# Performance work log

Measured on AMD Instinct MI355X. Metric: run time of the kernel, lower is better.

## Reference

```python
import math
import jax, jax.numpy as jnp
import numpy as np


def _alibi_slopes(n):
    def pow2_slopes(n):
        start = 2.0 ** (-(2.0 ** (-(math.log2(n) - 3))))
        return [start * (start ** i) for i in range(n)]
    if math.log2(n).is_integer():
        return pow2_slopes(n)
    cp2 = 2 ** math.floor(math.log2(n))
    return pow2_slopes(cp2) + _alibi_slopes(2 * cp2)[0::2][: n - cp2]


NUM_HEADS = 16


def setup_inputs() -> dict:
    key = jax.random.key(0)
    ks = jax.random.split(key, 5)
    B, S, H = 2, 2048, 2048
    return {
        "hidden_states": jax.random.normal(ks[0], (B, S, H), jnp.float32),
        "w_qkv": jax.random.normal(ks[1], (H, 3 * H), jnp.float32) * (H ** -0.5),
        "b_qkv": jax.random.normal(ks[2], (3 * H,), jnp.float32) * 0.02,
        "w_proj": jax.random.normal(ks[3], (H, H), jnp.float32) * (H ** -0.5),
        "b_proj": jax.random.normal(ks[4], (H,), jnp.float32) * 0.02,
    }


def reference(hidden_states, w_qkv, b_qkv, w_proj, b_proj):
    B, S, H = hidden_states.shape
    nh = NUM_HEADS
    hd = H // nh
    scale = 1.0 / hd  # mup scale_qk_dot_by_d=True -> d^-1 (not d^-0.5)

    qkv = hidden_states @ w_qkv + b_qkv  # [B,S,3H]
    q, k, v = jnp.split(qkv, 3, axis=-1)
    q = q.reshape(B, S, nh, hd)
    k = k.reshape(B, S, nh, hd)
    v = v.reshape(B, S, nh, hd)

    scores = jnp.einsum("bqhd,bkhd->bhqk", q, k) * scale  # [B,nh,S,S]

    slopes = jnp.asarray(_alibi_slopes(nh), dtype=scores.dtype)  # [nh]
    pos = jnp.arange(S)
    rel = (pos[None, :] - pos[:, None]).astype(scores.dtype)  # j - i, <=0 in causal region
    bias = slopes[:, None, None] * rel[None, :, :]  # [nh,S,S]
    causal = pos[None, :] <= pos[:, None]  # [S,S]

    scores = jnp.where(causal[None, None], scores + bias[None], jnp.finfo(scores.dtype).min)
    attn = jax.nn.softmax(scores, axis=-1)

    out = jnp.einsum("bhqk,bkhd->bqhd", attn, v).reshape(B, S, H)
    return out @ w_proj + b_proj
```

## Files before the change

### kernel.cpp

```cpp
#include <hip/hip_runtime.h>
#include <hip/hip_bf16.h>

typedef short bf16x8 __attribute__((ext_vector_type(8)));
typedef float f32x4 __attribute__((ext_vector_type(4)));
typedef unsigned short ushort_t;

#define NH 16
#define HD 128
#define SEQ 2048
#define HID 2048
#define NQKV 6144
#define BATCH 2

__device__ __forceinline__ ushort_t f2bf(float x) {
    unsigned u = __builtin_bit_cast(unsigned, x);
    u = (u + 0x7fffu + ((u >> 16) & 1u)) >> 16;
    return (ushort_t)u;
}

__device__ __forceinline__ void gl2lds16(const ushort_t* g, ushort_t* l) {
    __builtin_amdgcn_global_load_lds(
        (__attribute__((address_space(1))) void*)(g),
        (__attribute__((address_space(3))) void*)(l), 16, 0, 0);
}

__global__ __launch_bounds__(256) void to_bf16(
    const float* __restrict__ x, ushort_t* __restrict__ y, int n8) {
    int i = blockIdx.x * 256 + threadIdx.x;
    if (i >= n8) return;
    float4 a0 = *(const float4*)(x + (size_t)i * 8);
    float4 a1 = *(const float4*)(x + (size_t)i * 8 + 4);
    union { ushort_t u[8]; uint4 v; } p;
    p.u[0]=f2bf(a0.x); p.u[1]=f2bf(a0.y); p.u[2]=f2bf(a0.z); p.u[3]=f2bf(a0.w);
    p.u[4]=f2bf(a1.x); p.u[5]=f2bf(a1.y); p.u[6]=f2bf(a1.z); p.u[7]=f2bf(a1.w);
    *(uint4*)(y + (size_t)i * 8) = p.v;
}

__global__ __launch_bounds__(256) void transpose_to_bf16(
    const float* __restrict__ w, ushort_t* __restrict__ wT, int K, int N) {
    __shared__ float tile[32][33];
    int nb = blockIdx.x * 32, kb = blockIdx.y * 32;
    int tx = threadIdx.x, ty = threadIdx.y;
#pragma unroll
    for (int i = 0; i < 4; ++i) {
        int k = kb + ty + i * 8;
        tile[ty + i * 8][tx] = w[(size_t)k * N + nb + tx];
    }
    __syncthreads();
#pragma unroll
    for (int i = 0; i < 4; ++i) {
        int n = nb + ty + i * 8;
        wT[(size_t)n * K + kb + tx] = f2bf(tile[tx][ty + i * 8]);
    }
}

#define GEMM_KLOOP(A_, BT_)                                                     \
    const int t = threadIdx.x;                                                  \
    const int w = t >> 6, lane = t & 63, lm = lane & 15, lq = lane >> 4;        \
    const int wm = (w >> 1) * 64, wn = (w & 1) * 64;                            \
    const int lrow = lane >> 3, lsw = (lane & 7) ^ lrow;                        \
    f32x4 acc[4][4] = {};                                                       \
    const ushort_t* gA = A_ + (size_t)(mb + w * 32 + lrow) * HID + lsw * 8;     \
    const ushort_t* gB = BT_ + (size_t)(nb + w * 32 + lrow) * HID + lsw * 8;    \
    for (int kb = 0; kb < HID; kb += 64) {                                      \
        __syncthreads();                                                        \
        _Pragma("unroll")                                                       \
        for (int c = 0; c < 4; ++c) {                                           \
            gl2lds16(gA + (size_t)c * 8 * HID + kb, At + (w * 256 + c * 64) * 8); \
            gl2lds16(gB + (size_t)c * 8 * HID + kb, Bt + (w * 256 + c * 64) * 8); \
        }                                                                       \
        __syncthreads();                                                        \
        _Pragma("unroll")                                                       \
        for (int kc = 0; kc < 2; ++kc) {                                        \
            const int slot = (kc * 4 + lq) ^ (lm & 7);                          \
            bf16x8 af[4], bfr[4];                                               \
            _Pragma("unroll")                                                   \
            for (int mt = 0; mt < 4; ++mt)                                      \
                af[mt] = ((const bf16x8*)At)[(wm + mt * 16 + lm) * 8 + slot];   \
            _Pragma("unroll")                                                   \
            for (int nt = 0; nt < 4; ++nt)                                      \
                bfr[nt] = ((const bf16x8*)Bt)[(wn + nt * 16 + lm) * 8 + slot];  \
            _Pragma("unroll")                                                   \
            for (int mt = 0; mt < 4; ++mt)                                      \
                _Pragma("unroll")                                               \
                for (int nt = 0; nt < 4; ++nt)                                  \
                    acc[mt][nt] = __builtin_amdgcn_mfma_f32_16x16x32_bf16(      \
                        af[mt], bfr[nt], acc[mt][nt], 0, 0, 0);                 \
        }                                                                       \
    }

__global__ __launch_bounds__(256) void gemm_qkv(
    const ushort_t* __restrict__ A, const ushort_t* __restrict__ BT,
    const float* __restrict__ bias,
    ushort_t* __restrict__ qbuf, ushort_t* __restrict__ kbuf,
    ushort_t* __restrict__ vTbuf) {
    __shared__ unsigned shbuf[128 * 68];
    ushort_t* At = (ushort_t*)shbuf;
    ushort_t* Bt = At + 128 * 64;
    const int mb = blockIdx.x * 128;
    const int nb = blockIdx.y * 128;
    GEMM_KLOOP(A, BT)

    const int sec = nb >> 11;
    if (sec < 2) {
#pragma unroll
        for (int mt = 0; mt < 4; ++mt)
#pragma unroll
            for (int nt = 0; nt < 4; ++nt)
#pragma unroll
                for (int r = 0; r < 4; ++r) {
                    int m = mb + wm + mt * 16 + lq * 4 + r;
                    int c = nb + wn + nt * 16 + lm;
                    float val = acc[mt][nt][r] + bias[c];
                    int h = (c >> 7) & 15;
                    int d = c & 127;
                    int b = m >> 11, s = m & 2047;
                    size_t bh = (size_t)(b * NH + h);
                    ushort_t* dst = (sec == 0) ? qbuf : kbuf;
                    dst[(bh * SEQ + s) * HD + d] = f2bf(val);
                }
    } else {
        __syncthreads();
        unsigned* T = shbuf;
#pragma unroll
        for (int mt = 0; mt < 4; ++mt)
#pragma unroll
            for (int nt = 0; nt < 4; ++nt) {
                const int cl = wn + nt * 16 + lm;
                const int ml = wm + mt * 16 + lq * 4;
                const float bb = bias[nb + cl];
#pragma unroll
                for (int r = 0; r < 4; r += 2) {
                    unsigned pk = (unsigned)f2bf(acc[mt][nt][r] + bb) |
                                  ((unsigned)f2bf(acc[mt][nt][r + 1] + bb) << 16);
                    T[cl * 68 + ((ml + r) >> 1)] = pk;
                }
            }
        __syncthreads();
        const int d = t & 127, sh = t >> 7;
        const int b = mb >> 11, sbase = mb & 2047;
        const int hv = (nb >> 7) - 32;
        ushort_t* vrow = vTbuf + ((size_t)(b * NH + hv) * HD + d) * SEQ + sbase + sh * 64;
#pragma unroll
        for (int i = 0; i < 8; ++i)
            *(uint4*)(vrow + i * 8) = *(const uint4*)&T[d * 68 + sh * 32 + i * 4];
    }
}

__global__ __launch_bounds__(256) void gemm_proj(
    const ushort_t* __restrict__ A, const ushort_t* __restrict__ BT,
    const float* __restrict__ bias, float* __restrict__ out) {
    __shared__ ushort_t Abuf[128 * 64];
    __shared__ ushort_t Bbuf[128 * 64];
    ushort_t* At = Abuf;
    ushort_t* Bt = Bbuf;
    const int mb = blockIdx.x * 128;
    const int nb = blockIdx.y * 128;
    GEMM_KLOOP(A, BT)
#pragma unroll
    for (int mt = 0; mt < 4; ++mt)
#pragma unroll
        for (int nt = 0; nt < 4; ++nt)
#pragma unroll
            for (int r = 0; r < 4; ++r) {
                int m = mb + wm + mt * 16 + lq * 4 + r;
                int c = nb + wn + nt * 16 + lm;
                out[(size_t)m * HID + c] = acc[mt][nt][r] + bias[c];
            }
}

__global__ __launch_bounds__(256) void attn_kernel(
    const ushort_t* __restrict__ qb, const ushort_t* __restrict__ kbuf,
    const ushort_t* __restrict__ vT, ushort_t* __restrict__ ob) {
    __shared__ ushort_t Ks[64 * 128];
    __shared__ ushort_t Vs[128 * 64];
    __shared__ ushort_t Ps[4][16 * 72];

    const int bid = blockIdx.x;
    const int x = bid & 7, g = bid >> 3;
    const int qt = 31 - (g >> 2);
    const int bh = ((g & 3) << 3) | x;
    const int qbase = qt * 64;
    const int t = threadIdx.x, w = t >> 6, lane = t & 63;
    const int lm = lane & 15, lq = lane >> 4;

    const ushort_t* Qg = qb + (size_t)bh * SEQ * HD;
    const ushort_t* Kg = kbuf + (size_t)bh * SEQ * HD;
    const ushort_t* Vg = vT + (size_t)bh * HD * SEQ;

    const float LOG2E = 1.44269504f;
    const int h = bh & 15;
    const float slope2 = exp2f(-0.5f * (float)(h + 1)) * LOG2E;
    const float scale2 = (1.0f / 128.0f) * LOG2E;

    const int qg = qbase + w * 16 + lm;

    bf16x8 qf[4];
#pragma unroll
    for (int kc = 0; kc < 4; ++kc) {
        uint4 qv = *(const uint4*)(Qg + (size_t)qg * HD + kc * 32 + lq * 8);
        qf[kc] = __builtin_bit_cast(bf16x8, qv);
    }

    float foff[4][4];
    int koff[4][4];
#pragma unroll
    for (int mt = 0; mt < 4; ++mt)
#pragma unroll
        for (int r = 0; r < 4; ++r) {
            koff[mt][r] = mt * 16 + lq * 4 + r;
            foff[mt][r] = slope2 * (float)koff[mt][r];
        }

    float mrow = -1e30f, lrow = 0.0f;
    f32x4 O[8] = {};
    const int nkt = qt + 1;

    for (int kt = 0; kt < nkt; ++kt) {
        __syncthreads();
        {
            const ushort_t* Kt = Kg + (size_t)kt * 64 * HD;
#pragma unroll
            for (int i = 0; i < 4; ++i) {
                int ci = i * 256 + t;
                int kr = ci >> 4, ks = ci & 15;
                int kcg = (ks & 8) | ((ks & 7) ^ (kr & 7));
                gl2lds16(Kt + (size_t)kr * HD + kcg * 8, Ks + (i * 256 + w * 64) * 8);
                int vr = ci >> 3, vs = ci & 7;
                int vcg = vs ^ (vr & 7);
                gl2lds16(Vg + (size_t)vr * SEQ + kt * 64 + vcg * 8, Vs + (i * 256 + w * 64) * 8);
            }
        }
        __syncthreads();

        f32x4 sacc[4] = {};
#pragma unroll
        for (int kc = 0; kc < 4; ++kc) {
            const int slot = ((kc * 4 + lq) & 8) | (((kc * 4 + lq) & 7) ^ (lm & 7));
#pragma unroll
            for (int mt = 0; mt < 4; ++mt) {
                bf16x8 bk = *(const bf16x8*)&Ks[((mt * 16 + lm) * 16 + slot) * 8];
                sacc[mt] = __builtin_amdgcn_mfma_f32_16x16x32_bf16(bk, qf[kc], sacc[mt], 0, 0, 0);
            }
        }

        const float sbase = slope2 * (float)(kt * 64 - qg);
        float sc[4][4];
        if (kt == qt) {
#pragma unroll
            for (int mt = 0; mt < 4; ++mt)
#pragma unroll
                for (int r = 0; r < 4; ++r) {
                    float s = sacc[mt][r] * scale2 + (sbase + foff[mt][r]);
                    sc[mt][r] = (kt * 64 + koff[mt][r] <= qg) ? s : -3e38f;
                }
        } else {
#pragma unroll
            for (int mt = 0; mt < 4; ++mt)
#pragma unroll
                for (int r = 0; r < 4; ++r)
                    sc[mt][r] = sacc[mt][r] * scale2 + (sbase + foff[mt][r]);
        }

        float tm = sc[0][0];
#pragma unroll
        for (int mt = 0; mt < 4; ++mt)
#pragma unroll
            for (int r = 0; r < 4; ++r) tm = fmaxf(tm, sc[mt][r]);
        tm = fmaxf(tm, __shfl_xor(tm, 16));
        tm = fmaxf(tm, __shfl_xor(tm, 32));
        float mnew = fmaxf(mrow, tm);
        float alpha = __builtin_amdgcn_exp2f(mrow - mnew);
        mrow = mnew;

        float psum = 0.0f;
#pragma unroll
        for (int mt = 0; mt < 4; ++mt) {
            float p0 = __builtin_amdgcn_exp2f(sc[mt][0] - mnew);
            float p1 = __builtin_amdgcn_exp2f(sc[mt][1] - mnew);
            float p2 = __builtin_amdgcn_exp2f(sc[mt][2] - mnew);
            float p3 = __builtin_amdgcn_exp2f(sc[mt][3] - mnew);
            psum += (p0 + p1) + (p2 + p3);
            uint2 wv;
            wv.x = ((unsigned)f2bf(p1) << 16) | f2bf(p0);
            wv.y = ((unsigned)f2bf(p3) << 16) | f2bf(p2);
            *(uint2*)&Ps[w][lm * 72 + mt * 16 + lq * 4] = wv;
        }
        psum += __shfl_xor(psum, 16);
        psum += __shfl_xor(psum, 32);
        lrow = lrow * alpha + psum;

        float av[4];
#pragma unroll
        for (int r = 0; r < 4; ++r) av[r] = __shfl(alpha, lq * 4 + r);
#pragma unroll
        for (int nt = 0; nt < 8; ++nt)
#pragma unroll
            for (int r = 0; r < 4; ++r) O[nt][r] *= av[r];

        asm volatile("s_waitcnt lgkmcnt(0)" ::: "memory");
#pragma unroll
        for (int kc2 = 0; kc2 < 2; ++kc2) {
            bf16x8 ap = *(const bf16x8*)&Ps[w][lm * 72 + kc2 * 32 + lq * 8];
            const int slot = (kc2 * 4 + lq) ^ (lm & 7);
#pragma unroll
            for (int nt = 0; nt < 8; ++nt) {
                bf16x8 bv = *(const bf16x8*)&Vs[((nt * 16 + lm) * 8 + slot) * 8];
                O[nt] = __builtin_amdgcn_mfma_f32_16x16x32_bf16(ap, bv, O[nt], 0, 0, 0);
            }
        }
    }

    float lb[4];
#pragma unroll
    for (int r = 0; r < 4; ++r)
        lb[r] = __builtin_amdgcn_rcpf(__shfl(lrow, lq * 4 + r));
    const int b = bh >> 4;
#pragma unroll
    for (int nt = 0; nt < 8; ++nt)
#pragma unroll
        for (int r = 0; r < 4; ++r) {
            int s = qbase + w * 16 + lq * 4 + r;
            int d = nt * 16 + lm;
            ob[((size_t)(b * SEQ + s)) * HID + h * HD + d] = f2bf(O[nt][r] * lb[r]);
        }
}

extern "C" void kernel_launch(void* const* d_in, const int* in_sizes, int n_in,
                              void* d_out, int out_size, void* d_ws, size_t ws_size,
                              hipStream_t stream) {
    const float* hidden = (const float*)d_in[0];
    const float* w_qkv = (const float*)d_in[1];
    const float* b_qkv = (const float*)d_in[2];
    const float* w_proj = (const float*)d_in[3];
    const float* b_proj = (const float*)d_in[4];
    float* out = (float*)d_out;

    char* ws = (char*)d_ws;
    size_t off = 0;
    ushort_t* wqkvT = (ushort_t*)(ws + off); off += (size_t)NQKV * HID * 2;
    ushort_t* wprojT = (ushort_t*)(ws + off); off += (size_t)HID * HID * 2;
    ushort_t* hbf = (ushort_t*)(ws + off); off += (size_t)BATCH * SEQ * HID * 2;
    ushort_t* qw = (ushort_t*)(ws + off); off += (size_t)BATCH * NH * SEQ * HD * 2;
    ushort_t* kw = (ushort_t*)(ws + off); off += (size_t)BATCH * NH * SEQ * HD * 2;
    ushort_t* vTw = (ushort_t*)(ws + off); off += (size_t)BATCH * NH * SEQ * HD * 2;
    ushort_t* attnw = (ushort_t*)(ws + off); off += (size_t)BATCH * SEQ * HID * 2;

    to_bf16<<<dim3(BATCH * SEQ * HID / 8 / 256), 256, 0, stream>>>(
        hidden, hbf, BATCH * SEQ * HID / 8);
    transpose_to_bf16<<<dim3(NQKV / 32, HID / 32), dim3(32, 8), 0, stream>>>(
        w_qkv, wqkvT, HID, NQKV);
    transpose_to_bf16<<<dim3(HID / 32, HID / 32), dim3(32, 8), 0, stream>>>(
        w_proj, wprojT, HID, HID);

    gemm_qkv<<<dim3(BATCH * SEQ / 128, NQKV / 128), 256, 0, stream>>>(
        hbf, wqkvT, b_qkv, qw, kw, vTw);

    attn_kernel<<<dim3(BATCH * NH * 32), 256, 0, stream>>>(qw, kw, vTw, attnw);

    gemm_proj<<<dim3(BATCH * SEQ / 128, HID / 128), 256, 0, stream>>>(
        attnw, wprojT, b_proj, out);
}
```

Baseline: 364.4 us.

## Register-prefetch next K/V tile, skip lazy rescale, raise MFMA priority

```diff
diff --git a/kernel.cpp b/kernel.cpp
--- a/kernel.cpp
+++ b/kernel.cpp
@@ -203,37 +203,57 @@
     }
 
     float foff[4][4];
-    int koff[4][4];
 #pragma unroll
     for (int mt = 0; mt < 4; ++mt)
 #pragma unroll
-        for (int r = 0; r < 4; ++r) {
-            koff[mt][r] = mt * 16 + lq * 4 + r;
-            foff[mt][r] = slope2 * (float)koff[mt][r];
-        }
+        for (int r = 0; r < 4; ++r)
+            foff[mt][r] = slope2 * (float)(mt * 16 + lq * 4 + r);
+
+    int koffs[4], voffs[4];
+#pragma unroll
+    for (int i = 0; i < 4; ++i) {
+        int ci = i * 256 + t;
+        int kr = ci >> 4, ks = ci & 15;
+        int kcg = (ks & 8) | ((ks & 7) ^ (kr & 7));
+        koffs[i] = kr * HD + kcg * 8;
+        int vr = ci >> 3, vs = ci & 7;
+        int vcg = vs ^ (vr & 7);
+        voffs[i] = vr * SEQ + vcg * 8;
+    }
 
     float mrow = -1e30f, lrow = 0.0f;
     f32x4 O[8] = {};
     const int nkt = qt + 1;
 
+    const ushort_t* Kt = Kg;
+    const ushort_t* Vt = Vg;
+    uint4 kreg[4], vreg[4];
+#pragma unroll
+    for (int i = 0; i < 4; ++i) {
+        kreg[i] = *(const uint4*)(Kt + koffs[i]);
+        vreg[i] = *(const uint4*)(Vt + voffs[i]);
+    }
+
     for (int kt = 0; kt < nkt; ++kt) {
         __syncthreads();
-        {
-            const ushort_t* Kt = Kg + (size_t)kt * 64 * HD;
+#pragma unroll
+        for (int i = 0; i < 4; ++i) {
+            *(uint4*)&Ks[(i * 256 + t) * 8] = kreg[i];
+            *(uint4*)&Vs[(i * 256 + t) * 8] = vreg[i];
+        }
+        if (kt + 1 < nkt) {
+            Kt += 64 * HD;
+            Vt += 64;
 #pragma unroll
             for (int i = 0; i < 4; ++i) {
-                int ci = i * 256 + t;
-                int kr = ci >> 4, ks = ci & 15;
-                int kcg = (ks & 8) | ((ks & 7) ^ (kr & 7));
-                gl2lds16(Kt + (size_t)kr * HD + kcg * 8, Ks + (i * 256 + w * 64) * 8);
-                int vr = ci >> 3, vs = ci & 7;
-                int vcg = vs ^ (vr & 7);
-                gl2lds16(Vg + (size_t)vr * SEQ + kt * 64 + vcg * 8, Vs + (i * 256 + w * 64) * 8);
+                kreg[i] = *(const uint4*)(Kt + koffs[i]);
+                vreg[i] = *(const uint4*)(Vt + voffs[i]);
             }
         }
         __syncthreads();
 
         f32x4 sacc[4] = {};
+        __builtin_amdgcn_s_setprio(1);
 #pragma unroll
         for (int kc = 0; kc < 4; ++kc) {
             const int slot = ((kc * 4 + lq) & 8) | (((kc * 4 + lq) & 7) ^ (lm & 7));
@@ -243,6 +263,7 @@
                 sacc[mt] = __builtin_amdgcn_mfma_f32_16x16x32_bf16(bk, qf[kc], sacc[mt], 0, 0, 0);
             }
         }
+        __builtin_amdgcn_s_setprio(0);
 
         const float sbase = slope2 * (float)(kt * 64 - qg);
         float sc[4][4];
@@ -252,7 +273,7 @@
 #pragma unroll
                 for (int r = 0; r < 4; ++r) {
                     float s = sacc[mt][r] * scale2 + (sbase + foff[mt][r]);
-                    sc[mt][r] = (kt * 64 + koff[mt][r] <= qg) ? s : -3e38f;
+                    sc[mt][r] = (kt * 64 + mt * 16 + lq * 4 + r <= qg) ? s : -3e38f;
                 }
         } else {
 #pragma unroll
@@ -269,8 +290,16 @@
             for (int r = 0; r < 4; ++r) tm = fmaxf(tm, sc[mt][r]);
         tm = fmaxf(tm, __shfl_xor(tm, 16));
         tm = fmaxf(tm, __shfl_xor(tm, 32));
-        float mnew = fmaxf(mrow, tm);
-        float alpha = __builtin_amdgcn_exp2f(mrow - mnew);
+
+        const bool noresc = __all(tm <= mrow + 8.0f) && (kt > 0);
+        float mnew, alpha;
+        if (noresc) {
+            mnew = mrow;
+            alpha = 1.0f;
+        } else {
+            mnew = fmaxf(mrow, tm);
+            alpha = __builtin_amdgcn_exp2f(mrow - mnew);
+        }
         mrow = mnew;
 
         float psum = 0.0f;
@@ -290,15 +319,18 @@
         psum += __shfl_xor(psum, 32);
         lrow = lrow * alpha + psum;
 
-        float av[4];
-#pragma unroll
-        for (int r = 0; r < 4; ++r) av[r] = __shfl(alpha, lq * 4 + r);
-#pragma unroll
-        for (int nt = 0; nt < 8; ++nt)
-#pragma unroll
-            for (int r = 0; r < 4; ++r) O[nt][r] *= av[r];
+        if (!noresc) {
+            float av[4];
+#pragma unroll
+            for (int r = 0; r < 4; ++r) av[r] = __shfl(alpha, lq * 4 + r);
+#pragma unroll
+            for (int nt = 0; nt < 8; ++nt)
+#pragma unroll
+                for (int r = 0; r < 4; ++r) O[nt][r] *= av[r];
+        }
 
         asm volatile("s_waitcnt lgkmcnt(0)" ::: "memory");
+        __builtin_amdgcn_s_setprio(1);
 #pragma unroll
         for (int kc2 = 0; kc2 < 2; ++kc2) {
             bf16x8 ap = *(const bf16x8*)&Ps[w][lm * 72 + kc2 * 32 + lq * 8];
@@ -309,6 +341,7 @@
                 O[nt] = __builtin_amdgcn_mfma_f32_16x16x32_bf16(ap, bv, O[nt], 0, 0, 0);
             }
         }
+        __builtin_amdgcn_s_setprio(0);
     }
 
     float lb[4];
```

Measured after the change: 467.2 us. 28.2% more time.
